# Kernel tuning notes

Hardware: AMD Instinct MI355X
Metric: run time of the kernel (lower is better)

## Reference

```python
import jax, jax.numpy as jnp
from jax import lax
import numpy as np

D = 512        # d_model
F = 128        # raw feature dim
MS = 1024      # logic (service) nodes
NP_ = 16384    # physical nodes
EL = 4096      # logic edges
EP = 131072    # phys edges
SRC = 0        # source_node_idx
NEG = -1e9


def _gnn(feats, edge_index, Win, Wout, N):
    row, col = edge_index
    h = jax.nn.relu(feats @ Win)                                  # [N, D]
    agg = jax.ops.segment_sum(h[row], col, num_segments=N)        # [N, D]
    return jax.nn.relu((h + agg) @ Wout)


def _bfs_hop(edge_index, N, src, iters=16):
    # BFS hop distance from src (bounded Bellman-Ford relaxation)
    row, col = edge_index
    big = jnp.int32(N)
    dist = jnp.full((N,), big, jnp.int32).at[src].set(0)
    def body(_, d):
        cand = jnp.minimum(d[row] + 1, big)
        upd = jax.ops.segment_min(cand, col, num_segments=N)
        return jnp.minimum(d, upd)
    return lax.fori_loop(0, iters, body, dist)


def _forward(logic_feats, phys_feats, Ws_in, Ws_out, Wp_in, Wp_out,
             sA1, sA2, pA1, pA2, Wq, Wk, Wc1, bc1, wc2,
             logic_edge_index, phys_edge_index, actions, static_mask, topo_order):
    Np = phys_feats.shape[0]
    cloud = Np - 1                                                # cloud_node_idx = -1
    h_s = _gnn(logic_feats, logic_edge_index, Ws_in, Ws_out, logic_feats.shape[0])
    h_p = _gnn(phys_feats, phys_edge_index, Wp_in, Wp_out, Np)
    # task-specific residual adapters
    h_s = h_s + jax.nn.relu(h_s @ sA1) @ sA2
    h_p = h_p + jax.nn.relu(h_p @ pA1) @ pA2
    metric = _bfs_hop(phys_edge_index, Np, SRC)                   # [Np] int32
    q_all = (h_s @ Wq) / jnp.sqrt(jnp.float32(D))                 # [Ms, D]
    K = h_p @ Wk                                                  # [Np, D]
    acts = actions.astype(jnp.int32)

    def step(state, i):
        visited, last, logp_sum, ent_sum, switches, relax = state
        base = static_mask[i]                                     # [Np] bool
        # cloud_sticky branch
        sticky = jnp.zeros_like(base).at[cloud].set(base[cloud])
        # forbid_return (allow_stay keeps `last`)
        forbid = visited.at[last].set(False)
        allowed_n = base & (~forbid) & (metric >= metric[last])   # metric_non_decreasing
        allowed = jnp.where(last == cloud, sticky, allowed_n)
        any_a = allowed.any()
        # relaxation fallback: stay -> cloud -> base
        fb_stay = jnp.zeros_like(base).at[last].set(True)
        fb_cloud = jnp.zeros_like(base).at[cloud].set(True)
        fallback = jnp.where(base[last], fb_stay, jnp.where(base[cloud], fb_cloud, base))
        allowed = jnp.where(any_a, allowed, fallback)
        # actor: masked categorical over physical nodes
        logits = K @ q_all[i]                                     # [Np]
        logp_all = jax.nn.log_softmax(jnp.where(allowed, logits, NEG))
        p = jnp.exp(logp_all)
        ent = -jnp.sum(p * logp_all)
        a = acts[i]
        ne = a != last
        visited = visited.at[last].set(visited[last] | ne)
        last = jnp.where(ne, a, last)
        return (visited, last, logp_sum + logp_all[a], ent_sum + ent,
                switches + ne.astype(jnp.int32), relax + (~any_a).astype(jnp.int32)), None

    init = (jnp.zeros((Np,), bool), jnp.int32(SRC),
            jnp.float32(0.0), jnp.float32(0.0), jnp.int32(0), jnp.int32(0))
    (visited, last, logp_sum, ent_sum, switches, relax), _ = lax.scan(
        step, init, topo_order.astype(jnp.int32))
    # value head
    pooled = jnp.concatenate([h_s.mean(0), h_p.mean(0)])          # [2D]
    value = jax.nn.relu(pooled @ Wc1 + bc1) @ wc2                 # scalar
    return jnp.stack([logp_sum, ent_sum, value])


def setup_inputs() -> dict:
    key = jax.random.key(0)
    ks = jax.random.split(key, 20)
    s = 0.05
    def w(k, shape):
        return jax.random.normal(k, shape, jnp.float32) * s
    return {
        "logic_edge_index": jax.random.randint(ks[0], (2, EL), 0, MS, jnp.int32),
        "logic_feats": jax.random.normal(ks[1], (MS, F), jnp.float32),
        "phys_edge_index": jax.random.randint(ks[2], (2, EP), 0, NP_, jnp.int32),
        "phys_feats": jax.random.normal(ks[3], (NP_, F), jnp.float32),
        "actions": jax.random.randint(ks[4], (MS,), 0, NP_, jnp.int32),
        "static_mask": jnp.ones((MS, NP_), bool),
        "topo_order": jnp.arange(MS, dtype=jnp.int32),
        "Ws_in": w(ks[5], (F, D)), "Ws_out": w(ks[6], (D, D)),
        "Wp_in": w(ks[7], (F, D)), "Wp_out": w(ks[8], (D, D)),
        "sA1": w(ks[9], (D, D)), "sA2": w(ks[10], (D, D)),
        "pA1": w(ks[11], (D, D)), "pA2": w(ks[12], (D, D)),
        "Wq": w(ks[13], (D, D)), "Wk": w(ks[14], (D, D)),
        "Wc1": w(ks[15], (2 * D, D)),
        "bc1": jnp.zeros((D,), jnp.float32),
        "wc2": w(ks[16], (D,)),
    }


def reference(logic_edge_index, logic_feats, phys_edge_index, phys_feats,
              actions, static_mask, topo_order,
              Ws_in, Ws_out, Wp_in, Wp_out, sA1, sA2, pA1, pA2,
              Wq, Wk, Wc1, bc1, wc2):
    return _forward(logic_feats, phys_feats, Ws_in, Ws_out, Wp_in, Wp_out,
                    sA1, sA2, pA1, pA2, Wq, Wk, Wc1, bc1, wc2,
                    logic_edge_index, phys_edge_index, actions, static_mask, topo_order)
```

## Files before the change

### kernel.cpp

```cpp
#include <hip/hip_runtime.h>
#include <cstdint>
#include <cstddef>

typedef __bf16 bf16_t;
typedef bf16_t bf16x8 __attribute__((ext_vector_type(8)));
typedef bf16_t bf16x4v __attribute__((ext_vector_type(4)));
typedef float f32x4 __attribute__((ext_vector_type(4)));

#define NEGV (-1e9f)

#define GLDS(gp, lp) __builtin_amdgcn_global_load_lds( \
    (const __attribute__((address_space(1))) void*)(gp), \
    (__attribute__((address_space(3))) void*)(lp), 16, 0, 0)

struct PrepArgs {
    const float* w512src[8]; bf16_t* w512dst[8];
    const float* w128src[2]; bf16_t* w128dst[2];
    const float* logicF; const float* physF;
    bf16_t* featsSb; bf16_t* featsPb;
    int* cntC; int* cntR; int* cntL; int* firstL; int* dist; float* pooled; float* hacc;
};

__global__ __launch_bounds__(256)
void k_prep(PrepArgs p) {
    __shared__ float tb[64][65];
    const int b = blockIdx.x, tid = threadIdx.x;
    if (b < 544) {
        const float* src; bf16_t* dst; int K, tile;
        if (b < 512) { src = p.w512src[b >> 6]; dst = p.w512dst[b >> 6]; K = 512; tile = b & 63; }
        else { int bb = b - 512; src = p.w128src[bb >> 4]; dst = p.w128dst[bb >> 4]; K = 128; tile = bb & 15; }
        const int N = 512;
        int kt = tile >> 3, tc = tile & 7;
        int cx = tid & 63, ry = tid >> 6;
#pragma unroll
        for (int q = 0; q < 16; ++q) {
            int r = q * 4 + ry;
            tb[r][cx] = src[(size_t)(kt * 64 + r) * N + tc * 64 + cx];
        }
        __syncthreads();
#pragma unroll
        for (int q = 0; q < 16; ++q) {
            int r2 = q * 4 + ry;
            dst[(size_t)(tc * 64 + r2) * K + kt * 64 + cx] = (bf16_t)tb[cx][r2];
        }
    } else if (b < 672) {
        size_t e0 = (size_t)(b - 544) * 1024 + tid * 4;
        float4 v = *(const float4*)(p.logicF + e0);
        bf16x4v o; o[0]=(bf16_t)v.x; o[1]=(bf16_t)v.y; o[2]=(bf16_t)v.z; o[3]=(bf16_t)v.w;
        *(bf16x4v*)(p.featsSb + e0) = o;
    } else if (b < 2720) {
        size_t e0 = (size_t)(b - 672) * 1024 + tid * 4;
        float4 v = *(const float4*)(p.physF + e0);
        bf16x4v o; o[0]=(bf16_t)v.x; o[1]=(bf16_t)v.y; o[2]=(bf16_t)v.z; o[3]=(bf16_t)v.w;
        *(bf16x4v*)(p.featsPb + e0) = o;
    } else {
        int gid = (b - 2720) * 256 + tid;
        p.cntC[gid] = 0; p.cntR[gid] = 0; p.firstL[gid] = 0x7fffffff;
        p.dist[gid] = (gid == 0) ? 0 : 16384;
        if (gid < 1024) { p.cntL[gid] = 0; p.pooled[gid] = 0.0f; }
        if (gid < 512) p.hacc[gid] = 0.0f;
    }
}

__global__ void k_hist3(const int* __restrict__ rowP, const int* __restrict__ colP,
                        const int* __restrict__ rowL, const int* __restrict__ colL,
                        int* cntC, int* cntR, int* cntL, int EP, int EL) {
    int e = blockIdx.x * 256 + threadIdx.x;
    if (e < EP) atomicAdd(&cntC[colP[e]], 1);
    else if (e < 2 * EP) atomicAdd(&cntR[rowP[e - EP]], 1);
    else if (e < 2 * EP + EL) atomicAdd(&cntL[colL[e - 2 * EP]], 1);
}

__global__ __launch_bounds__(256)
void k_scan3(int* cntC, int* offC, int* curC,
             int* cntR, int* offR, int* curR,
             int* cntL, int* offL, int* curL) {
    __shared__ int ss[256];
    int tid = threadIdx.x;
    const int* cnt; int* off; int* cur; int n;
    if (blockIdx.x == 0)      { cnt = cntC; off = offC; cur = curC; n = 16384; }
    else if (blockIdx.x == 1) { cnt = cntR; off = offR; cur = curR; n = 16384; }
    else                      { cnt = cntL; off = offL; cur = curL; n = 1024; }
    int chunk = n / 256, base = tid * chunk, s = 0;
    for (int i = 0; i < chunk; ++i) s += cnt[base + i];
    ss[tid] = s; __syncthreads();
    for (int d = 1; d < 256; d <<= 1) {
        int v = (tid >= d) ? ss[tid - d] : 0;
        __syncthreads(); ss[tid] += v; __syncthreads();
    }
    int run = (tid == 0) ? 0 : ss[tid - 1];
    for (int i = 0; i < chunk; ++i) { off[base + i] = run; cur[base + i] = run; run += cnt[base + i]; }
    if (tid == 255) off[n] = run;
}

__global__ void k_scatter3(const int* __restrict__ rowP, const int* __restrict__ colP,
                           const int* __restrict__ rowL, const int* __restrict__ colL,
                           int* curC, int* curR, int* curL,
                           int* erowCP, int* ecolRP, int* erowL, int EP, int EL) {
    int e = blockIdx.x * 256 + threadIdx.x;
    if (e < EP) {
        int c = colP[e]; int q = atomicAdd(&curC[c], 1); erowCP[q] = rowP[e];
    } else if (e < 2 * EP) {
        int e2 = e - EP;
        int c = rowP[e2]; int q = atomicAdd(&curR[c], 1); ecolRP[q] = colP[e2];
    } else if (e < 2 * EP + EL) {
        int e3 = e - 2 * EP;
        int c = colL[e3]; int q = atomicAdd(&curL[c], 1); erowL[q] = rowL[e3];
    }
}

__global__ void k_traj(const int* __restrict__ topo, const int* __restrict__ acts,
                       int* __restrict__ lastArr, int* __restrict__ first_left, int MSn, int src) {
    int s = blockIdx.x * 256 + threadIdx.x;
    if (s < MSn) {
        int last = (s == 0) ? src : acts[topo[s - 1]];
        lastArr[s] = last;
        int a = acts[topo[s]];
        if (a != last) atomicMin(&first_left[last], s);
    }
}

__global__ __launch_bounds__(256)
void k_bfs_level(const int* __restrict__ offR, const int* __restrict__ ecol,
                 int* __restrict__ dist, int lev) {
    int j = blockIdx.x * 256 + threadIdx.x;
    if (dist[j] != lev) return;
    int e0 = offR[j], e1 = offR[j + 1];
    for (int e = e0; e < e1; ++e) {
        int v = ecol[e];
        if (dist[v] == 16384) dist[v] = lev + 1;
    }
}

__global__ __launch_bounds__(256)
void k_fmpack(const int* __restrict__ firstL, const int* __restrict__ dist, int* __restrict__ fm) {
    int j = blockIdx.x * 256 + threadIdx.x;
    int fl = firstL[j]; if (fl > 0xFFFF) fl = 0xFFFF;
    fm[j] = (fl << 16) | dist[j];
}

__global__ void k_pack_mask(const int* __restrict__ m, uint32_t* __restrict__ bits) {
    size_t w = (size_t)blockIdx.x * 256 + threadIdx.x;
    const int4* p = (const int4*)(m + w * 32);
    uint32_t b = 0;
#pragma unroll
    for (int q = 0; q < 8; ++q) {
        int4 v = p[q];
        b |= (v.x != 0 ? 1u : 0u) << (q * 4);
        b |= (v.y != 0 ? 1u : 0u) << (q * 4 + 1);
        b |= (v.z != 0 ? 1u : 0u) << (q * 4 + 2);
        b |= (v.w != 0 ? 1u : 0u) << (q * 4 + 3);
    }
    bits[w] = b;
}

struct GemmDesc { const bf16_t* A; const bf16_t* B; const bf16_t* Cin; bf16_t* O;
                  int N; int K; float scale; int relu; };
struct GemmPair { GemmDesc d0; GemmDesc d1; int split; };

__global__ __launch_bounds__(256)
void gemm_mfma(GemmPair args) {
    __shared__ bf16_t As[2][128 * 32];
    __shared__ bf16_t Bs[2][128 * 32];
    const int inSet1 = (blockIdx.y >= args.split);
    const GemmDesc g = inSet1 ? args.d1 : args.d0;
    const int my = blockIdx.y - (inSet1 ? args.split : 0);
    const int m0 = my * 128, n0 = blockIdx.x * 128;
    const int tid = threadIdx.x, wave = tid >> 6, lane = tid & 63;
    const int wm = (wave >> 1) * 64, wn = (wave & 1) * 64;
    const int lr = lane & 15, lk = (lane >> 4) * 8;
    const int K = g.K;
    const int srr = wave * 16 + (lane >> 2);
    const int scb = (((lane & 3) ^ ((lane >> 2) & 3)) << 4);
    const char* Abase = (const char*)g.A + ((size_t)(m0 + srr) * K) * 2 + scb;
    const char* Bbase = (const char*)g.B + ((size_t)(n0 + srr) * K) * 2 + scb;
    const size_t rstep = (size_t)64 * K * 2;
    f32x4 acc[4][4] = {};

    auto stage = [&](int q, int k0) {
        const char* a0 = Abase + (size_t)k0 * 2;
        const char* b0 = Bbase + (size_t)k0 * 2;
        GLDS(a0,         &As[q][(wave * 16) * 32]);
        GLDS(a0 + rstep, &As[q][(64 + wave * 16) * 32]);
        GLDS(b0,         &Bs[q][(wave * 16) * 32]);
        GLDS(b0 + rstep, &Bs[q][(64 + wave * 16) * 32]);
    };

    stage(0, 0);
    asm volatile("s_waitcnt vmcnt(0)" ::: "memory");
    __syncthreads();
    const int nt = K >> 5;
    for (int t = 0; t < nt; ++t) {
        int cur = t & 1;
        if (t + 1 < nt) stage(cur ^ 1, (t + 1) << 5);
        bf16x8 af[4], bff[4];
#pragma unroll
        for (int mi = 0; mi < 4; ++mi) {
            int r = wm + mi * 16 + lr;
            int pb = r * 64 + ((lk * 2) ^ ((r & 3) << 4));
            af[mi] = *(const bf16x8*)((const char*)&As[cur][0] + pb);
        }
#pragma unroll
        for (int ni = 0; ni < 4; ++ni) {
            int r = wn + ni * 16 + lr;
            int pb = r * 64 + ((lk * 2) ^ ((r & 3) << 4));
            bff[ni] = *(const bf16x8*)((const char*)&Bs[cur][0] + pb);
        }
#pragma unroll
        for (int mi = 0; mi < 4; ++mi)
#pragma unroll
            for (int ni = 0; ni < 4; ++ni)
                acc[mi][ni] = __builtin_amdgcn_mfma_f32_16x16x32_bf16(af[mi], bff[ni], acc[mi][ni], 0, 0, 0);
        asm volatile("s_waitcnt vmcnt(0)" ::: "memory");
        __syncthreads();
    }
    const int rb = m0 + wm + (lane >> 4) * 4;
    const int cb = n0 + wn + lr;
#pragma unroll
    for (int mi = 0; mi < 4; ++mi)
#pragma unroll
        for (int ni = 0; ni < 4; ++ni)
#pragma unroll
            for (int r = 0; r < 4; ++r) {
                int row = rb + mi * 16 + r;
                int col = cb + ni * 16;
                size_t idx = (size_t)row * g.N + col;
                float v = acc[mi][ni][r] * g.scale;
                if (g.Cin) v += (float)g.Cin[idx];
                if (g.relu) v = fmaxf(v, 0.0f);
                g.O[idx] = (bf16_t)v;
            }
}

__global__ __launch_bounds__(256)
void k_spmm2(const bf16_t* __restrict__ HL, const int* __restrict__ offL, const int* __restrict__ erowL, bf16_t* __restrict__ XL,
             const bf16_t* __restrict__ HP, const int* __restrict__ offP, const int* __restrict__ erowP, bf16_t* __restrict__ XP) {
    int b = blockIdx.x;
    const bf16_t* H; const int* off; const int* erow; bf16_t* X; int c;
    int wib = threadIdx.x >> 6, lane = threadIdx.x & 63;
    if (b < 256) { H = HL; off = offL; erow = erowL; X = XL; c = b * 4 + wib; }
    else { b -= 256; H = HP; off = offP; erow = erowP; X = XP; c = b * 4 + wib; }
    int d0 = lane * 8;
    float acc[8] = {0,0,0,0,0,0,0,0};
    int e0 = off[c], e1 = off[c + 1];
    for (int e = e0; e < e1; ++e) {
        int r = erow[e];
        bf16x8 h = *(const bf16x8*)(H + (size_t)r * 512 + d0);
#pragma unroll
        for (int j = 0; j < 8; ++j) acc[j] += (float)h[j];
    }
    bf16x8 own = *(const bf16x8*)(H + (size_t)c * 512 + d0);
    bf16x8 o;
#pragma unroll
    for (int j = 0; j < 8; ++j) o[j] = (bf16_t)((float)own[j] + acc[j]);
    *(bf16x8*)(X + (size_t)c * 512 + d0) = o;
}

__global__ __launch_bounds__(256)
void k_scan2(const bf16_t* __restrict__ S, const uint32_t* __restrict__ bits,
             const int* __restrict__ fm, const int* __restrict__ topo,
             const int* __restrict__ acts, const int* __restrict__ lastA,
             float* __restrict__ slogp, float* __restrict__ sent) {
    const int NPn = 16384, cloud = NPn - 1;
    __shared__ float msh[256], zsh[256], wsh[256];
    __shared__ int ash[256];
    const int s = blockIdx.x, tid = threadIdx.x;
    const int i = topo[s], a = acts[i], last = lastA[s];
    const bf16_t* Srow = S + (size_t)i * NPn;
    const uint32_t* brow = bits + (size_t)i * 512;
    const int ml = fm[last] & 0xFFFF;
    const int baseCloud = (brow[511] >> 31) & 1;
    const int lic = (last == cloud);
    if (lic && baseCloud) {
        if (tid == 0) {
            float M = (float)Srow[cloud];
            slogp[s] = (a == cloud) ? 0.0f : (NEGV - M);
            sent[s] = 0.0f;
        }
        return;
    }
    float m = -3.4e38f, Z = 0.0f, W = 0.0f;
    int any = 0;
    if (!lic) {
        for (int c = 0; c < 8; ++c) {
            int j0 = c * 2048 + tid * 8;
            bf16x8 sv = *(const bf16x8*)(Srow + j0);
            uint32_t b8 = (brow[j0 >> 5] >> (j0 & 24)) & 0xFFu;
            int4 f0 = *(const int4*)(fm + j0);
            int4 f1 = *(const int4*)(fm + j0 + 4);
            int fj[8] = {f0.x, f0.y, f0.z, f0.w, f1.x, f1.y, f1.z, f1.w};
#pragma unroll
            for (int q = 0; q < 8; ++q) {
                int j = j0 + q;
                bool alw = ((b8 >> q) & 1) && ((fj[q] & 0xFFFF) >= ml)
                           && (j == last || (((unsigned)fj[q]) >> 16) >= (unsigned)s);
                if (alw) {
                    any = 1;
                    float l = (float)sv[q];
                    if (l > m) {
                        float d = m - l, ce = expf(d);
                        W = ce * (W + d * Z);
                        Z = ce * Z + 1.0f;
                        m = l;
                    } else {
                        float t = l - m, e = expf(t);
                        Z += e; W += t * e;
                    }
                }
            }
        }
    }
    msh[tid] = m; zsh[tid] = Z; wsh[tid] = W; ash[tid] = any;
    __syncthreads();
    for (int st = 128; st > 0; st >>= 1) {
        if (tid < st) {
            float m1 = msh[tid], Z1 = zsh[tid], W1 = wsh[tid];
            float m2 = msh[tid + st], Z2 = zsh[tid + st], W2 = wsh[tid + st];
            float M2 = fmaxf(m1, m2);
            float e1 = expf(m1 - M2), e2 = expf(m2 - M2);
            zsh[tid] = e1 * Z1 + e2 * Z2;
            wsh[tid] = e1 * (W1 + (m1 - M2) * Z1) + e2 * (W2 + (m2 - M2) * Z2);
            msh[tid] = M2;
            ash[tid] |= ash[tid + st];
        }
        __syncthreads();
    }
    if (tid != 0) return;
    if (ash[0]) {
        float M = msh[0], Zt = zsh[0], Wt = wsh[0];
        float logZ = logf(Zt);
        int fa = fm[a];
        bool alwa = ((brow[a >> 5] >> (a & 31)) & 1) && ((fa & 0xFFFF) >= ml)
                    && (a == last || (((unsigned)fa) >> 16) >= (unsigned)s);
        float la = alwa ? (float)Srow[a] : NEGV;
        slogp[s] = la - M - logZ;
        sent[s] = logZ - Wt / Zt;
        return;
    }
    int baseLast = (brow[last >> 5] >> (last & 31)) & 1;
    if (baseLast) { float M = (float)Srow[last]; slogp[s] = (a == last) ? 0.0f : (NEGV - M); sent[s] = 0.0f; return; }
    if (baseCloud) { float M = (float)Srow[cloud]; slogp[s] = (a == cloud) ? 0.0f : (NEGV - M); sent[s] = 0.0f; return; }
    float mm = -3.4e38f, ZZ = 0.0f, WW = 0.0f;
    for (int j = 0; j < NPn; ++j) {
        if ((brow[j >> 5] >> (j & 31)) & 1) {
            float l = (float)Srow[j];
            if (l > mm) { float d = mm - l, ce = expf(d); WW = ce * (WW + d * ZZ); ZZ = ce * ZZ + 1.0f; mm = l; }
            else { float t = l - mm, e = expf(t); ZZ += e; WW += t * e; }
        }
    }
    if (ZZ == 0.0f) { slogp[s] = -logf((float)NPn); sent[s] = logf((float)NPn); return; }
    float logZ = logf(ZZ);
    int ba = (brow[a >> 5] >> (a & 31)) & 1;
    float la = ba ? (float)Srow[a] : NEGV;
    slogp[s] = la - mm - logZ;
    sent[s] = logZ - WW / ZZ;
}

__global__ __launch_bounds__(256)
void k_pool2(const bf16_t* __restrict__ HL, const bf16_t* __restrict__ HP, float* __restrict__ pooled) {
    int b = blockIdx.x, tid = threadIdx.x;
    const bf16_t* H; float* dst; int R, bb, ng; float inv;
    if (b < 16) { H = HL; dst = pooled; R = 1024; inv = 1.0f / 1024.0f; bb = b; ng = 16; }
    else { H = HP; dst = pooled + 512; R = 16384; inv = 1.0f / 16384.0f; bb = b - 16; ng = 128; }
    float a0 = 0, a1 = 0;
    for (int r = bb; r < R; r += ng) {
        a0 += (float)H[(size_t)r * 512 + tid];
        a1 += (float)H[(size_t)r * 512 + tid + 256];
    }
    atomicAdd(&dst[tid], a0 * inv);
    atomicAdd(&dst[tid + 256], a1 * inv);
}

__global__ __launch_bounds__(256)
void k_vpart(const float* __restrict__ pooled, const float* __restrict__ Wc1, float* __restrict__ hacc) {
    __shared__ float pk[128];
    int b = blockIdx.x, tid = threadIdx.x;
    int k0 = b * 128;
    if (tid < 128) pk[tid] = pooled[k0 + tid];
    __syncthreads();
    float a0 = 0, a1 = 0;
    for (int kk = 0; kk < 128; ++kk) {
        float pv = pk[kk];
        const float* wr = Wc1 + (size_t)(k0 + kk) * 512;
        a0 += pv * wr[tid];
        a1 += pv * wr[tid + 256];
    }
    atomicAdd(&hacc[tid], a0);
    atomicAdd(&hacc[tid + 256], a1);
}

__global__ __launch_bounds__(256)
void k_epilogue(const float* __restrict__ slogp, const float* __restrict__ sent,
                const float* __restrict__ hacc, const float* __restrict__ bc1,
                const float* __restrict__ wc2, float* __restrict__ out) {
    __shared__ float s1[256], s2[256], s3[256];
    int tid = threadIdx.x;
    float a = 0, b = 0;
    for (int k = tid; k < 1024; k += 256) { a += slogp[k]; b += sent[k]; }
    float v = fmaxf(hacc[tid] + bc1[tid], 0.0f) * wc2[tid]
            + fmaxf(hacc[tid + 256] + bc1[tid + 256], 0.0f) * wc2[tid + 256];
    s1[tid] = a; s2[tid] = b; s3[tid] = v;
    __syncthreads();
    for (int st = 128; st > 0; st >>= 1) {
        if (tid < st) { s1[tid] += s1[tid + st]; s2[tid] += s2[tid + st]; s3[tid] += s3[tid + st]; }
        __syncthreads();
    }
    if (tid == 0) { out[0] = s1[0]; out[1] = s2[0]; out[2] = s3[0]; }
}

extern "C" void kernel_launch(void* const* d_in, const int* in_sizes, int n_in,
                              void* d_out, int out_size, void* d_ws, size_t ws_size,
                              hipStream_t stream) {
    (void)n_in; (void)out_size; (void)ws_size; (void)in_sizes;
    const int MS = 1024, NP = 16384, EL = 4096, EP = 131072, D = 512;
    const int SRCN = 0;

    const int* logicE = (const int*)d_in[0];
    const float* logicF = (const float*)d_in[1];
    const int* physE = (const int*)d_in[2];
    const float* physF = (const float*)d_in[3];
    const int* acts = (const int*)d_in[4];
    const int* mask = (const int*)d_in[5];
    const int* topo = (const int*)d_in[6];
    const float* Ws_in = (const float*)d_in[7];
    const float* Ws_out = (const float*)d_in[8];
    const float* Wp_in = (const float*)d_in[9];
    const float* Wp_out = (const float*)d_in[10];
    const float* sA1 = (const float*)d_in[11];
    const float* sA2 = (const float*)d_in[12];
    const float* pA1 = (const float*)d_in[13];
    const float* pA2 = (const float*)d_in[14];
    const float* Wq = (const float*)d_in[15];
    const float* Wk = (const float*)d_in[16];
    const float* Wc1 = (const float*)d_in[17];
    const float* bc1 = (const float*)d_in[18];
    const float* wc2 = (const float*)d_in[19];
    float* out = (float*)d_out;

    char* wsb = (char*)d_ws;
    size_t off = 0;
    auto alloc = [&](size_t bytes) -> void* {
        off = (off + 255) & ~(size_t)255;
        void* p = wsb + off; off += bytes; return p;
    };

    bf16_t* S_bf    = (bf16_t*)alloc((size_t)MS * NP * 2);
    bf16_t* PB0     = (bf16_t*)alloc((size_t)NP * D * 2);
    bf16_t* PB1     = (bf16_t*)alloc((size_t)NP * D * 2);
    bf16_t* PB2     = (bf16_t*)alloc((size_t)NP * D * 2);
    bf16_t* LB0     = (bf16_t*)alloc((size_t)MS * D * 2);
    bf16_t* LB1     = (bf16_t*)alloc((size_t)MS * D * 2);
    bf16_t* LB2     = (bf16_t*)alloc((size_t)MS * D * 2);
    bf16_t* featsSb = (bf16_t*)alloc((size_t)MS * 128 * 2);
    bf16_t* featsPb = (bf16_t*)alloc((size_t)NP * 128 * 2);
    bf16_t* WsinT   = (bf16_t*)alloc(512 * 128 * 2);
    bf16_t* WpinT   = (bf16_t*)alloc(512 * 128 * 2);
    bf16_t* WsoutT  = (bf16_t*)alloc(512 * 512 * 2);
    bf16_t* sA1T    = (bf16_t*)alloc(512 * 512 * 2);
    bf16_t* sA2T    = (bf16_t*)alloc(512 * 512 * 2);
    bf16_t* WqT     = (bf16_t*)alloc(512 * 512 * 2);
    bf16_t* WpoutT  = (bf16_t*)alloc(512 * 512 * 2);
    bf16_t* pA1T    = (bf16_t*)alloc(512 * 512 * 2);
    bf16_t* pA2T    = (bf16_t*)alloc(512 * 512 * 2);
    bf16_t* WkT     = (bf16_t*)alloc(512 * 512 * 2);
    int* cntC  = (int*)alloc(NP * 4);
    int* offC  = (int*)alloc((NP + 1) * 4);
    int* curC  = (int*)alloc(NP * 4);
    int* cntR  = (int*)alloc(NP * 4);
    int* offR  = (int*)alloc((NP + 1) * 4);
    int* curR  = (int*)alloc(NP * 4);
    int* cntL  = (int*)alloc(MS * 4);
    int* offL  = (int*)alloc((MS + 1) * 4);
    int* curL  = (int*)alloc(MS * 4);
    int* erowCP = (int*)alloc(EP * 4);
    int* ecolRP = (int*)alloc(EP * 4);
    int* erowL  = (int*)alloc(EL * 4);
    int* firstL = (int*)alloc(NP * 4);
    int* lastA  = (int*)alloc(MS * 4);
    int* dist   = (int*)alloc(NP * 4);
    int* fm     = (int*)alloc(NP * 4);
    float* slogp = (float*)alloc(MS * 4);
    float* sentb = (float*)alloc(MS * 4);
    float* pooled = (float*)alloc(1024 * 4);
    float* hacc   = (float*)alloc(512 * 4);
    uint32_t* bits = (uint32_t*)PB0;

    const int* rowP = physE;  const int* colP = physE + EP;
    const int* rowL = logicE; const int* colL = logicE + EL;

    {
        PrepArgs p;
        const float* s512[8] = {Ws_out, sA1, sA2, Wq, Wp_out, pA1, pA2, Wk};
        bf16_t* d512[8] = {WsoutT, sA1T, sA2T, WqT, WpoutT, pA1T, pA2T, WkT};
        for (int q = 0; q < 8; ++q) { p.w512src[q] = s512[q]; p.w512dst[q] = d512[q]; }
        p.w128src[0] = Ws_in; p.w128dst[0] = WsinT;
        p.w128src[1] = Wp_in; p.w128dst[1] = WpinT;
        p.logicF = logicF; p.physF = physF; p.featsSb = featsSb; p.featsPb = featsPb;
        p.cntC = cntC; p.cntR = cntR; p.cntL = cntL; p.firstL = firstL; p.dist = dist;
        p.pooled = pooled; p.hacc = hacc;
        hipLaunchKernelGGL(k_prep, dim3(2784), dim3(256), 0, stream, p);
    }
    hipLaunchKernelGGL(k_hist3, dim3((2 * EP + EL) / 256), dim3(256), 0, stream,
                       rowP, colP, rowL, colL, cntC, cntR, cntL, EP, EL);
    hipLaunchKernelGGL(k_scan3, dim3(3), dim3(256), 0, stream,
                       cntC, offC, curC, cntR, offR, curR, cntL, offL, curL);
    hipLaunchKernelGGL(k_scatter3, dim3((2 * EP + EL) / 256), dim3(256), 0, stream,
                       rowP, colP, rowL, colL, curC, curR, curL, erowCP, ecolRP, erowL, EP, EL);
    hipLaunchKernelGGL(k_traj, dim3(4), dim3(256), 0, stream, topo, acts, lastA, firstL, MS, SRCN);
    for (int lev = 0; lev < 16; ++lev)
        hipLaunchKernelGGL(k_bfs_level, dim3(64), dim3(256), 0, stream, offR, ecolRP, dist, lev);
    hipLaunchKernelGGL(k_fmpack, dim3(64), dim3(256), 0, stream, firstL, dist, fm);

    auto gemm2 = [&](const bf16_t* A0, const bf16_t* B0, const bf16_t* C0, bf16_t* O0, float sc0,
                     const bf16_t* A1, const bf16_t* B1, const bf16_t* C1, bf16_t* O1, float sc1,
                     int K, int relu) {
        GemmPair gp;
        gp.d0 = {A0, B0, C0, O0, 512, K, sc0, relu};
        gp.d1 = {A1, B1, C1, O1, 512, K, sc1, relu};
        gp.split = 8;
        hipLaunchKernelGGL(gemm_mfma, dim3(4, 136), dim3(256), 0, stream, gp);
    };

    gemm2(featsSb, WsinT, nullptr, LB0, 1.0f, featsPb, WpinT, nullptr, PB0, 1.0f, 128, 1);
    hipLaunchKernelGGL(k_spmm2, dim3(256 + 4096), dim3(256), 0, stream,
                       LB0, offL, erowL, LB1, PB0, offC, erowCP, PB1);
    gemm2(LB1, WsoutT, nullptr, LB0, 1.0f, PB1, WpoutT, nullptr, PB0, 1.0f, 512, 1);
    gemm2(LB0, sA1T, nullptr, LB1, 1.0f, PB0, pA1T, nullptr, PB1, 1.0f, 512, 1);
    gemm2(LB1, sA2T, LB0, LB2, 1.0f, PB1, pA2T, PB0, PB2, 1.0f, 512, 0);
    hipLaunchKernelGGL(k_pack_mask, dim3((MS * NP / 32) / 256), dim3(256), 0, stream, mask, bits);
    hipLaunchKernelGGL(k_pool2, dim3(144), dim3(256), 0, stream, LB2, PB2, pooled);
    gemm2(LB2, WqT, nullptr, LB1, 0.044194173824159216f, PB2, WkT, nullptr, PB1, 1.0f, 512, 0);
    {
        GemmPair gp;
        gp.d0 = {LB1, PB1, nullptr, S_bf, NP, 512, 1.0f, 0};
        gp.d1 = gp.d0;
        gp.split = 1000;
        hipLaunchKernelGGL(gemm_mfma, dim3(128, 8), dim3(256), 0, stream, gp);
    }
    hipLaunchKernelGGL(k_scan2, dim3(MS), dim3(256), 0, stream,
                       S_bf, bits, fm, topo, acts, lastA, slogp, sentb);
    hipLaunchKernelGGL(k_vpart, dim3(8), dim3(256), 0, stream, pooled, Wc1, hacc);
    hipLaunchKernelGGL(k_epilogue, dim3(1), dim3(256), 0, stream, slogp, sentb, hacc, bc1, wc2, out);
}
```

Baseline: 397.7 us.

## Replace per-level BFS launches with cooperative grid-synced kernel and merge small kernels

Replaces the 16 per-level BFS launches plus the fm pack kernel with a single cooperative kernel that uses grid.sync between levels and exits early once a level discovers no new node. The trajectory kernel is folded into the histogram launch and mask bit-packing is folded into the prep kernel, with bits given its own buffer. The aim is to cut kernel launch count and serialization gaps. In exchange it adds grid-wide barriers and atomics on dist, and depends on cooperative launch support.

```diff
diff --git a/kernel.cpp b/kernel.cpp
--- a/kernel.cpp
+++ b/kernel.cpp
@@ -1,4 +1,5 @@
 #include <hip/hip_runtime.h>
+#include <hip/hip_cooperative_groups.h>
 #include <cstdint>
 #include <cstddef>
 
@@ -18,7 +19,9 @@
     const float* w128src[2]; bf16_t* w128dst[2];
     const float* logicF; const float* physF;
     bf16_t* featsSb; bf16_t* featsPb;
-    int* cntC; int* cntR; int* cntL; int* firstL; int* dist; float* pooled; float* hacc;
+    const int* mask; uint32_t* bits;
+    int* cntC; int* cntR; int* cntL; int* firstL; int* dist; int* flags;
+    float* pooled; float* hacc;
 };
 
 __global__ __launch_bounds__(256)
@@ -53,22 +56,47 @@
         float4 v = *(const float4*)(p.physF + e0);
         bf16x4v o; o[0]=(bf16_t)v.x; o[1]=(bf16_t)v.y; o[2]=(bf16_t)v.z; o[3]=(bf16_t)v.w;
         *(bf16x4v*)(p.featsPb + e0) = o;
-    } else {
+    } else if (b < 2784) {
         int gid = (b - 2720) * 256 + tid;
         p.cntC[gid] = 0; p.cntR[gid] = 0; p.firstL[gid] = 0x7fffffff;
         p.dist[gid] = (gid == 0) ? 0 : 16384;
         if (gid < 1024) { p.cntL[gid] = 0; p.pooled[gid] = 0.0f; }
         if (gid < 512) p.hacc[gid] = 0.0f;
+        if (gid < 16) p.flags[gid] = 0;
+    } else {
+        size_t w = (size_t)(b - 2784) * 256 + tid;
+        const int4* q4 = (const int4*)(p.mask + w * 32);
+        uint32_t bb = 0;
+#pragma unroll
+        for (int q = 0; q < 8; ++q) {
+            int4 v = q4[q];
+            bb |= (v.x != 0 ? 1u : 0u) << (q * 4);
+            bb |= (v.y != 0 ? 1u : 0u) << (q * 4 + 1);
+            bb |= (v.z != 0 ? 1u : 0u) << (q * 4 + 2);
+            bb |= (v.w != 0 ? 1u : 0u) << (q * 4 + 3);
+        }
+        p.bits[w] = bb;
     }
 }
 
 __global__ void k_hist3(const int* __restrict__ rowP, const int* __restrict__ colP,
                         const int* __restrict__ rowL, const int* __restrict__ colL,
-                        int* cntC, int* cntR, int* cntL, int EP, int EL) {
-    int e = blockIdx.x * 256 + threadIdx.x;
-    if (e < EP) atomicAdd(&cntC[colP[e]], 1);
-    else if (e < 2 * EP) atomicAdd(&cntR[rowP[e - EP]], 1);
-    else if (e < 2 * EP + EL) atomicAdd(&cntL[colL[e - 2 * EP]], 1);
+                        int* cntC, int* cntR, int* cntL, int EP, int EL,
+                        const int* __restrict__ topo, const int* __restrict__ acts,
+                        int* __restrict__ lastArr, int* __restrict__ firstL) {
+    int b = blockIdx.x;
+    if (b < 1040) {
+        int e = b * 256 + threadIdx.x;
+        if (e < EP) atomicAdd(&cntC[colP[e]], 1);
+        else if (e < 2 * EP) atomicAdd(&cntR[rowP[e - EP]], 1);
+        else if (e < 2 * EP + EL) atomicAdd(&cntL[colL[e - 2 * EP]], 1);
+    } else {
+        int s = (b - 1040) * 256 + threadIdx.x;
+        int last = (s == 0) ? 0 : acts[topo[s - 1]];
+        lastArr[s] = last;
+        int a = acts[topo[s]];
+        if (a != last) atomicMin(&firstL[last], s);
+    }
 }
 
 __global__ __launch_bounds__(256)
@@ -109,49 +137,30 @@
     }
 }
 
-__global__ void k_traj(const int* __restrict__ topo, const int* __restrict__ acts,
-                       int* __restrict__ lastArr, int* __restrict__ first_left, int MSn, int src) {
-    int s = blockIdx.x * 256 + threadIdx.x;
-    if (s < MSn) {
-        int last = (s == 0) ? src : acts[topo[s - 1]];
-        lastArr[s] = last;
-        int a = acts[topo[s]];
-        if (a != last) atomicMin(&first_left[last], s);
-    }
-}
-
-__global__ __launch_bounds__(256)
-void k_bfs_level(const int* __restrict__ offR, const int* __restrict__ ecol,
-                 int* __restrict__ dist, int lev) {
-    int j = blockIdx.x * 256 + threadIdx.x;
-    if (dist[j] != lev) return;
-    int e0 = offR[j], e1 = offR[j + 1];
-    for (int e = e0; e < e1; ++e) {
-        int v = ecol[e];
-        if (dist[v] == 16384) dist[v] = lev + 1;
-    }
-}
-
-__global__ __launch_bounds__(256)
-void k_fmpack(const int* __restrict__ firstL, const int* __restrict__ dist, int* __restrict__ fm) {
-    int j = blockIdx.x * 256 + threadIdx.x;
+__global__ __launch_bounds__(256)
+void k_bfs_coop(const int* __restrict__ offR, const int* __restrict__ ecol,
+                const int* __restrict__ firstL, int* __restrict__ dist,
+                int* __restrict__ flags, int* __restrict__ fm) {
+    cooperative_groups::grid_group grid = cooperative_groups::this_grid();
+    const int j = blockIdx.x * 256 + threadIdx.x;
+    int dj = dist[j];
+    for (int lev = 0; lev < 16; ++lev) {
+        if (dj == 16384) dj = atomicAdd(&dist[j], 0);
+        if (dj == lev) {
+            int e0 = offR[j], e1 = offR[j + 1];
+            int found = 0;
+            for (int e = e0; e < e1; ++e) {
+                int old = atomicMin(&dist[ecol[e]], lev + 1);
+                found |= (old == 16384);
+            }
+            if (found) atomicExch(&flags[lev], 1);
+        }
+        grid.sync();
+        if (atomicAdd(&flags[lev], 0) == 0) break;
+    }
+    if (dj == 16384) dj = atomicAdd(&dist[j], 0);
     int fl = firstL[j]; if (fl > 0xFFFF) fl = 0xFFFF;
-    fm[j] = (fl << 16) | dist[j];
-}
-
-__global__ void k_pack_mask(const int* __restrict__ m, uint32_t* __restrict__ bits) {
-    size_t w = (size_t)blockIdx.x * 256 + threadIdx.x;
-    const int4* p = (const int4*)(m + w * 32);
-    uint32_t b = 0;
-#pragma unroll
-    for (int q = 0; q < 8; ++q) {
-        int4 v = p[q];
-        b |= (v.x != 0 ? 1u : 0u) << (q * 4);
-        b |= (v.y != 0 ? 1u : 0u) << (q * 4 + 1);
-        b |= (v.z != 0 ? 1u : 0u) << (q * 4 + 2);
-        b |= (v.w != 0 ? 1u : 0u) << (q * 4 + 3);
-    }
-    bits[w] = b;
+    fm[j] = (fl << 16) | dj;
 }
 
 struct GemmDesc { const bf16_t* A; const bf16_t* B; const bf16_t* Cin; bf16_t* O;
@@ -413,7 +422,6 @@
                               hipStream_t stream) {
     (void)n_in; (void)out_size; (void)ws_size; (void)in_sizes;
     const int MS = 1024, NP = 16384, EL = 4096, EP = 131072, D = 512;
-    const int SRCN = 0;
 
     const int* logicE = (const int*)d_in[0];
     const float* logicF = (const float*)d_in[1];
@@ -463,6 +471,7 @@
     bf16_t* pA1T    = (bf16_t*)alloc(512 * 512 * 2);
     bf16_t* pA2T    = (bf16_t*)alloc(512 * 512 * 2);
     bf16_t* WkT     = (bf16_t*)alloc(512 * 512 * 2);
+    uint32_t* bits = (uint32_t*)alloc((size_t)MS * NP / 8);
     int* cntC  = (int*)alloc(NP * 4);
     int* offC  = (int*)alloc((NP + 1) * 4);
     int* curC  = (int*)alloc(NP * 4);
@@ -479,11 +488,11 @@
     int* lastA  = (int*)alloc(MS * 4);
     int* dist   = (int*)alloc(NP * 4);
     int* fm     = (int*)alloc(NP * 4);
+    int* flags  = (int*)alloc(16 * 4);
     float* slogp = (float*)alloc(MS * 4);
     float* sentb = (float*)alloc(MS * 4);
     float* pooled = (float*)alloc(1024 * 4);
     float* hacc   = (float*)alloc(512 * 4);
-    uint32_t* bits = (uint32_t*)PB0;
 
     const int* rowP = physE;  const int* colP = physE + EP;
     const int* rowL = logicE; const int* colL = logicE + EL;
@@ -496,20 +505,23 @@
         p.w128src[0] = Ws_in; p.w128dst[0] = WsinT;
         p.w128src[1] = Wp_in; p.w128dst[1] = WpinT;
         p.logicF = logicF; p.physF = physF; p.featsSb = featsSb; p.featsPb = featsPb;
+        p.mask = mask; p.bits = bits;
         p.cntC = cntC; p.cntR = cntR; p.cntL = cntL; p.firstL = firstL; p.dist = dist;
-        p.pooled = pooled; p.hacc = hacc;
-        hipLaunchKernelGGL(k_prep, dim3(2784), dim3(256), 0, stream, p);
-    }
-    hipLaunchKernelGGL(k_hist3, dim3((2 * EP + EL) / 256), dim3(256), 0, stream,
-                       rowP, colP, rowL, colL, cntC, cntR, cntL, EP, EL);
+        p.flags = flags; p.pooled = pooled; p.hacc = hacc;
+        hipLaunchKernelGGL(k_prep, dim3(4832), dim3(256), 0, stream, p);
+    }
+    hipLaunchKernelGGL(k_hist3, dim3(1044), dim3(256), 0, stream,
+                       rowP, colP, rowL, colL, cntC, cntR, cntL, EP, EL,
+                       topo, acts, lastA, firstL);
     hipLaunchKernelGGL(k_scan3, dim3(3), dim3(256), 0, stream,
                        cntC, offC, curC, cntR, offR, curR, cntL, offL, curL);
     hipLaunchKernelGGL(k_scatter3, dim3((2 * EP + EL) / 256), dim3(256), 0, stream,
                        rowP, colP, rowL, colL, curC, curR, curL, erowCP, ecolRP, erowL, EP, EL);
-    hipLaunchKernelGGL(k_traj, dim3(4), dim3(256), 0, stream, topo, acts, lastA, firstL, MS, SRCN);
-    for (int lev = 0; lev < 16; ++lev)
-        hipLaunchKernelGGL(k_bfs_level, dim3(64), dim3(256), 0, stream, offR, ecolRP, dist, lev);
-    hipLaunchKernelGGL(k_fmpack, dim3(64), dim3(256), 0, stream, firstL, dist, fm);
+    {
+        void* bargs[6] = {(void*)&offR, (void*)&ecolRP, (void*)&firstL,
+                          (void*)&dist, (void*)&flags, (void*)&fm};
+        hipLaunchCooperativeKernel((const void*)k_bfs_coop, dim3(64), dim3(256), bargs, 0, stream);
+    }
 
     auto gemm2 = [&](const bf16_t* A0, const bf16_t* B0, const bf16_t* C0, bf16_t* O0, float sc0,
                      const bf16_t* A1, const bf16_t* B1, const bf16_t* C1, bf16_t* O1, float sc1,
@@ -527,7 +539,6 @@
     gemm2(LB1, WsoutT, nullptr, LB0, 1.0f, PB1, WpoutT, nullptr, PB0, 1.0f, 512, 1);
     gemm2(LB0, sA1T, nullptr, LB1, 1.0f, PB0, pA1T, nullptr, PB1, 1.0f, 512, 1);
     gemm2(LB1, sA2T, LB0, LB2, 1.0f, PB1, pA2T, PB0, PB2, 1.0f, 512, 0);
-    hipLaunchKernelGGL(k_pack_mask, dim3((MS * NP / 32) / 256), dim3(256), 0, stream, mask, bits);
     hipLaunchKernelGGL(k_pool2, dim3(144), dim3(256), 0, stream, LB2, PB2, pooled);
     gemm2(LB2, WqT, nullptr, LB1, 0.044194173824159216f, PB2, WkT, nullptr, PB1, 1.0f, 512, 0);
     {
```

Result: slower. 513.0 us (+29.0%).
